# Optimization experiments

Hardware: AMD Instinct MI355X
Metric: run time of the kernel (lower is better)

## Reference

```python
import jax, jax.numpy as jnp
import numpy as np

IN_CH, OUT_CH, KH, KW = 512, 512, 3, 3
LR_MULT = 1.0
WEIGHT_SCALE = LR_MULT / np.sqrt(IN_CH * KH * KW)


def setup_inputs() -> dict:
    key = jax.random.key(0)
    k1, k2, k3 = jax.random.split(key, 3)
    x = jax.random.normal(k1, (16, IN_CH, 32, 32), dtype=jnp.float32)
    s = jax.random.normal(k2, (16, IN_CH), dtype=jnp.float32)
    weight = jax.random.normal(k3, (OUT_CH, IN_CH, KH, KW), dtype=jnp.float32) / LR_MULT
    return {"x": x, "s": s, "weight": weight}


def reference(x, s, weight):
    B, Cin, H, Wd = x.shape
    Cout = weight.shape[0]
    W = weight * WEIGHT_SCALE                          # [Cout, Cin, kH, kW]
    # per-sample modulation: [B, Cout, Cin, kH, kW]
    Wm = s[:, None, :, None, None] * W[None]
    # demodulation: normalize each (b, out_channel) filter
    sigma = jnp.sqrt(jnp.sum(Wm ** 2, axis=(-3, -2, -1), keepdims=True) + 1e-8)
    Wm = Wm / sigma
    # grouped conv with groups = B
    x_g = x.reshape(1, B * Cin, H, Wd)
    W_g = Wm.reshape(B * Cout, Cin, KH, KW)
    out = jax.lax.conv_general_dilated(
        x_g, W_g,
        window_strides=(1, 1),
        padding="SAME",
        rhs_dilation=(1, 1),
        feature_group_count=B,
        dimension_numbers=("NCHW", "OIHW", "NCHW"),
    )
    return out.reshape(B, Cout, out.shape[-2], out.shape[-1])
```

## Files before the change

kernel.cpp:

```cpp
#include <hip/hip_runtime.h>
#include <hip/hip_bf16.h>


typedef __attribute__((ext_vector_type(4))) float f32x4;
typedef __attribute__((ext_vector_type(8))) short bf16x8;

#define NB    16
#define CIN   512
#define COUT  512
#define KTOT  4608
#define NPIX  (NB * 32 * 32)
#define BUFELEM 24576

#define WAITV6() asm volatile("s_waitcnt vmcnt(6)" ::: "memory")
#define WAITV0() asm volatile("s_waitcnt vmcnt(0)" ::: "memory")
#define FENCE()  asm volatile("" ::: "memory")
#define BAR()    { FENCE(); __builtin_amdgcn_s_barrier(); FENCE(); }

__device__ __forceinline__ void gload_lds16(const void* g, void* l) {
  __builtin_amdgcn_global_load_lds(
      (__attribute__((address_space(1))) void*)(g),
      (__attribute__((address_space(3))) void*)(l), 16, 0, 0);
}

__global__ __launch_bounds__(256) void pack_w_kernel(
    const float* __restrict__ w, __hip_bfloat16* __restrict__ wB,
    float* __restrict__ wsq) {
  const int idx = blockIdx.x * 256 + threadIdx.x;
  const int o = idx >> 9, ci = idx & 511;
  const float* wp = w + (size_t)idx * 9;
  const float WSCALE = 0.014731391274719739f;
  float sum = 0.f;
#pragma unroll
  for (int t = 0; t < 9; ++t) {
    float v = wp[t] * WSCALE;
    sum += v * v;
    wB[(size_t)o * KTOT + t * 512 + ci] = __float2bfloat16(v);
  }
  wsq[idx] = sum;
}

__global__ __launch_bounds__(256) void calc_rsig_kernel(
    const float* __restrict__ s, const float* __restrict__ wsq,
    float* __restrict__ rsig) {
  const int wid = blockIdx.x * 4 + (threadIdx.x >> 6);
  const int lane = threadIdx.x & 63;
  const int b = wid >> 9, o = wid & 511;
  const float* sp = s + b * 512;
  const float* wp = wsq + o * 512;
  float sum = 0.f;
#pragma unroll
  for (int i = 0; i < 8; ++i) {
    float sv = sp[lane + i * 64];
    sum += sv * sv * wp[lane + i * 64];
  }
#pragma unroll
  for (int off = 32; off > 0; off >>= 1) sum += __shfl_down(sum, off, 64);
  if (lane == 0) rsig[wid] = 1.0f / sqrtf(sum + 1e-8f);
}

__global__ __launch_bounds__(256) void modulate_kernel(
    const float* __restrict__ x, const float* __restrict__ s,
    __hip_bfloat16* __restrict__ xpad) {
  const int by = blockIdx.x;
  const int b = by >> 5, y = by & 31;
  __shared__ __attribute__((aligned(16))) __hip_bfloat16 tile[32][72];
  const int tid = threadIdx.x;
  const int xc = tid & 31;
  const int cr0 = tid >> 5;
  const float* xrow = x + ((size_t)b * 512 * 32 + y) * 32;
  const float* sb = s + b * 512;
  __hip_bfloat16* orow = xpad + (size_t)((b * 34 + y + 1) * 34) * 512;

  for (int ci0 = 0; ci0 < 512; ci0 += 64) {
#pragma unroll
    for (int r = 0; r < 8; ++r) {
      const int cir = r * 8 + cr0;
      const int ci = ci0 + cir;
      float v = xrow[(size_t)ci * 1024 + xc] * sb[ci];
      tile[xc][cir] = __float2bfloat16(v);
    }
    __syncthreads();
    const int xcw = tid >> 3, vec = tid & 7;
    bf16x8 v = *(const bf16x8*)&tile[xcw][vec * 8];
    *(bf16x8*)(orow + (size_t)(xcw + 1) * 512 + ci0 + vec * 8) = v;
    __syncthreads();
  }
}

__global__ __launch_bounds__(512, 1) void conv_gemm_kernel(
    const __hip_bfloat16* __restrict__ wB,
    const __hip_bfloat16* __restrict__ xpad,
    const float* __restrict__ rsig,
    float* __restrict__ out) {
  extern __shared__ __attribute__((aligned(16))) __hip_bfloat16 lds[];

  const int tid = threadIdx.x;
  const int wv = tid >> 6, lane = tid & 63;
  const int bo0 = blockIdx.y << 7;
  const int bp0 = blockIdx.x << 8;
  const int wr = wv >> 2, wc = wv & 3;

  int gA[2];
#pragma unroll
  for (int r = 0; r < 2; ++r) {
    const int c = r * 512 + tid, row = c >> 3, sc = (c & 7) ^ (row & 7);
    gA[r] = (bo0 + row) * KTOT + sc * 8;
  }
  int gB[4];
#pragma unroll
  for (int r = 0; r < 4; ++r) {
    const int c = r * 512 + tid, row = c >> 3, sc = (c & 7) ^ (row & 7);
    const int p = bp0 + row, b = p >> 10, rem = p & 1023, y = rem >> 5,
              xx = rem & 31;
    gB[r] = ((b * 34 + y) * 34 + xx) * 512 + sc * 8;
  }

  auto stageA = [&](int kt2, int r) {
    __hip_bfloat16* dst = lds + (kt2 % 3) * BUFELEM + (size_t)(r * 512 + (wv << 6)) * 8;
    gload_lds16(wB + (size_t)(gA[r] + (kt2 << 6)), dst);
  };
  auto stageB = [&](int kt2, int r, int xoff) {
    __hip_bfloat16* dst = lds + (kt2 % 3) * BUFELEM + 8192 + (size_t)(r * 512 + (wv << 6)) * 8;
    gload_lds16(xpad + (size_t)(gB[r] + xoff), dst);
  };

  f32x4 acc[4][4];
#pragma unroll
  for (int mi = 0; mi < 4; ++mi)
#pragma unroll
    for (int ni = 0; ni < 4; ++ni) acc[mi][ni] = f32x4{0.f, 0.f, 0.f, 0.f};

  stageA(0, 0); stageA(0, 1);
  stageB(0, 0, 0); stageB(0, 1, 0); stageB(0, 2, 0); stageB(0, 3, 0);
  stageA(1, 0); stageA(1, 1);
  stageB(1, 0, 64); stageB(1, 1, 64); stageB(1, 2, 64); stageB(1, 3, 64);
  WAITV6();
  BAR();

  for (int kt = 0; kt < 72; ++kt) {
    const __hip_bfloat16* bufA = lds + (kt % 3) * BUFELEM;
    const __hip_bfloat16* bufB = bufA + 8192;
    const int kt2 = kt + 2;
    const bool pf = kt2 < 72;
    int xoff = 0;
    if (pf) {
      const int tap = kt2 >> 3, ty = (tap * 11) >> 5;
      xoff = (tap + 31 * ty) * 512 + ((kt2 & 7) << 6);
    }

    {
      bf16x8 af[4], bv[4];
      const int kb = (lane >> 4) << 4;
#pragma unroll
      for (int mi = 0; mi < 4; ++mi) {
        const int row = (wr << 6) + (mi << 4) + (lane & 15);
        af[mi] = *(const bf16x8*)((const char*)bufA + row * 128 +
                                  (kb ^ ((row & 7) << 4)));
      }
#pragma unroll
      for (int ni = 0; ni < 4; ++ni) {
        const int row = (wc << 6) + (ni << 4) + (lane & 15);
        bv[ni] = *(const bf16x8*)((const char*)bufB + row * 128 +
                                  (kb ^ ((row & 7) << 4)));
      }
      if (pf) { stageA(kt2, 0); stageA(kt2, 1); stageB(kt2, 0, xoff); }
      BAR();
      __builtin_amdgcn_s_setprio(1);
#pragma unroll
      for (int mi = 0; mi < 4; ++mi)
#pragma unroll
        for (int ni = 0; ni < 4; ++ni)
          acc[mi][ni] = __builtin_amdgcn_mfma_f32_16x16x32_bf16(
              af[mi], bv[ni], acc[mi][ni], 0, 0, 0);
      __builtin_amdgcn_s_setprio(0);
      BAR();
    }

    {
      bf16x8 af[4], bv[4];
      const int kb = 64 + ((lane >> 4) << 4);
#pragma unroll
      for (int mi = 0; mi < 4; ++mi) {
        const int row = (wr << 6) + (mi << 4) + (lane & 15);
        af[mi] = *(const bf16x8*)((const char*)bufA + row * 128 +
                                  (kb ^ ((row & 7) << 4)));
      }
#pragma unroll
      for (int ni = 0; ni < 4; ++ni) {
        const int row = (wc << 6) + (ni << 4) + (lane & 15);
        bv[ni] = *(const bf16x8*)((const char*)bufB + row * 128 +
                                  (kb ^ ((row & 7) << 4)));
      }
      if (pf) { stageB(kt2, 1, xoff); stageB(kt2, 2, xoff); stageB(kt2, 3, xoff); }
      BAR();
      __builtin_amdgcn_s_setprio(1);
#pragma unroll
      for (int mi = 0; mi < 4; ++mi)
#pragma unroll
        for (int ni = 0; ni < 4; ++ni)
          acc[mi][ni] = __builtin_amdgcn_mfma_f32_16x16x32_bf16(
              af[mi], bv[ni], acc[mi][ni], 0, 0, 0);
      __builtin_amdgcn_s_setprio(0);
      if (kt < 70) { WAITV6(); } else if (kt == 70) { WAITV0(); }
      BAR();
    }
  }

  const int bimg = bp0 >> 10;
#pragma unroll
  for (int mi = 0; mi < 4; ++mi) {
    const int o = bo0 + (wr << 6) + (mi << 4) + ((lane >> 4) << 2);
    const f32x4 rs = *(const f32x4*)(rsig + (bimg << 9) + o);
#pragma unroll
    for (int ni = 0; ni < 4; ++ni) {
      const int p = bp0 + (wc << 6) + (ni << 4) + (lane & 15);
      const int prem = p & 1023;
#pragma unroll
      for (int r = 0; r < 4; ++r)
        out[((size_t)(bimg << 9) + o + r) * 1024 + prem] =
            acc[mi][ni][r] * rs[r];
    }
  }
}

extern "C" void kernel_launch(void* const* d_in, const int* in_sizes, int n_in,
                              void* d_out, int out_size, void* d_ws,
                              size_t ws_size, hipStream_t stream) {
  const float* x = (const float*)d_in[0];
  const float* s = (const float*)d_in[1];
  const float* w = (const float*)d_in[2];
  float* out = (float*)d_out;

  char* ws = (char*)d_ws;
  const size_t xpad_bytes = (size_t)NB * 34 * 34 * 512 * 2;
  const size_t wB_bytes = (size_t)COUT * KTOT * 2;
  const size_t wsq_bytes = (size_t)COUT * CIN * 4;
  __hip_bfloat16* xpad = (__hip_bfloat16*)ws;
  __hip_bfloat16* wB = (__hip_bfloat16*)(ws + xpad_bytes);
  float* wsq = (float*)(ws + xpad_bytes + wB_bytes);
  float* rsig = (float*)(ws + xpad_bytes + wB_bytes + wsq_bytes);

  const int lds_bytes = 3 * BUFELEM * 2;
  hipFuncSetAttribute((const void*)conv_gemm_kernel,
                      hipFuncAttributeMaxDynamicSharedMemorySize, lds_bytes);

  hipMemsetAsync(xpad, 0, xpad_bytes, stream);
  pack_w_kernel<<<(COUT * CIN) / 256, 256, 0, stream>>>(w, wB, wsq);
  modulate_kernel<<<NB * 32, 256, 0, stream>>>(x, s, xpad);
  calc_rsig_kernel<<<(NB * COUT) / 4, 256, 0, stream>>>(s, wsq, rsig);
  conv_gemm_kernel<<<dim3(NPIX / 256, COUT / 128), 512, lds_bytes, stream>>>(
      wB, xpad, rsig, out);
}
```

Baseline: 108.9 us.

## Split GEMM k-tile into four quadrant phases with interleaved LDS reads and prefetch

Each k-tile iteration of the conv GEMM is restructured from two half-K phases into four output-quadrant phases. Each phase loads both K halves of the fragments it needs, issues part of the next tile's global-to-LDS prefetch, then waits on lgkmcnt and runs its MFMAs behind a scheduling barrier. The aim is to overlap LDS fragment reads and prefetch issue with MFMA work at finer granularity. Launch bounds also change to request two blocks per CU, which caps registers even though LDS use likely still allows only one block; this adds barriers per iteration and risks register spills.

```diff
diff --git a/kernel.cpp b/kernel.cpp
--- a/kernel.cpp
+++ b/kernel.cpp
@@ -10,10 +10,13 @@
 #define COUT  512
 #define KTOT  4608
 #define NPIX  (NB * 32 * 32)
+#define KTILES 72
 #define BUFELEM 24576
 
 #define WAITV6() asm volatile("s_waitcnt vmcnt(6)" ::: "memory")
 #define WAITV0() asm volatile("s_waitcnt vmcnt(0)" ::: "memory")
+#define LGKM0()  asm volatile("s_waitcnt lgkmcnt(0)" ::: "memory")
+#define SCHED0() __builtin_amdgcn_sched_barrier(0)
 #define FENCE()  asm volatile("" ::: "memory")
 #define BAR()    { FENCE(); __builtin_amdgcn_s_barrier(); FENCE(); }
 
@@ -88,7 +91,7 @@
   }
 }
 
-__global__ __launch_bounds__(512, 1) void conv_gemm_kernel(
+__global__ __launch_bounds__(512, 2) void conv_gemm_kernel(
     const __hip_bfloat16* __restrict__ wB,
     const __hip_bfloat16* __restrict__ xpad,
     const float* __restrict__ rsig,
@@ -138,73 +141,103 @@
   WAITV6();
   BAR();
 
-  for (int kt = 0; kt < 72; ++kt) {
+#pragma unroll 1
+  for (int kt = 0; kt < KTILES; ++kt) {
     const __hip_bfloat16* bufA = lds + (kt % 3) * BUFELEM;
     const __hip_bfloat16* bufB = bufA + 8192;
     const int kt2 = kt + 2;
-    const bool pf = kt2 < 72;
+    const bool pf = kt2 < KTILES;
     int xoff = 0;
     if (pf) {
-      const int tap = kt2 >> 3, ty = (tap * 11) >> 5;
-      xoff = (tap + 31 * ty) * 512 + ((kt2 & 7) << 6);
-    }
-
-    {
-      bf16x8 af[4], bv[4];
-      const int kb = (lane >> 4) << 4;
-#pragma unroll
-      for (int mi = 0; mi < 4; ++mi) {
-        const int row = (wr << 6) + (mi << 4) + (lane & 15);
-        af[mi] = *(const bf16x8*)((const char*)bufA + row * 128 +
-                                  (kb ^ ((row & 7) << 4)));
-      }
-#pragma unroll
-      for (int ni = 0; ni < 4; ++ni) {
-        const int row = (wc << 6) + (ni << 4) + (lane & 15);
-        bv[ni] = *(const bf16x8*)((const char*)bufB + row * 128 +
-                                  (kb ^ ((row & 7) << 4)));
-      }
-      if (pf) { stageA(kt2, 0); stageA(kt2, 1); stageB(kt2, 0, xoff); }
-      BAR();
-      __builtin_amdgcn_s_setprio(1);
-#pragma unroll
-      for (int mi = 0; mi < 4; ++mi)
-#pragma unroll
-        for (int ni = 0; ni < 4; ++ni)
-          acc[mi][ni] = __builtin_amdgcn_mfma_f32_16x16x32_bf16(
-              af[mi], bv[ni], acc[mi][ni], 0, 0, 0);
-      __builtin_amdgcn_s_setprio(0);
-      BAR();
-    }
-
-    {
-      bf16x8 af[4], bv[4];
-      const int kb = 64 + ((lane >> 4) << 4);
-#pragma unroll
-      for (int mi = 0; mi < 4; ++mi) {
-        const int row = (wr << 6) + (mi << 4) + (lane & 15);
-        af[mi] = *(const bf16x8*)((const char*)bufA + row * 128 +
-                                  (kb ^ ((row & 7) << 4)));
-      }
-#pragma unroll
-      for (int ni = 0; ni < 4; ++ni) {
-        const int row = (wc << 6) + (ni << 4) + (lane & 15);
-        bv[ni] = *(const bf16x8*)((const char*)bufB + row * 128 +
-                                  (kb ^ ((row & 7) << 4)));
-      }
-      if (pf) { stageB(kt2, 1, xoff); stageB(kt2, 2, xoff); stageB(kt2, 3, xoff); }
-      BAR();
-      __builtin_amdgcn_s_setprio(1);
-#pragma unroll
-      for (int mi = 0; mi < 4; ++mi)
-#pragma unroll
-        for (int ni = 0; ni < 4; ++ni)
-          acc[mi][ni] = __builtin_amdgcn_mfma_f32_16x16x32_bf16(
-              af[mi], bv[ni], acc[mi][ni], 0, 0, 0);
-      __builtin_amdgcn_s_setprio(0);
-      if (kt < 70) { WAITV6(); } else if (kt == 70) { WAITV0(); }
-      BAR();
-    }
+      const int tap = kt2 >> 3;
+      xoff = (tap + 31 * (tap / 3)) * 512 + ((kt2 & 7) << 6);
+    }
+
+    bf16x8 af[4][2], bv[4][2];
+    const int kbase = (lane >> 4) << 4;
+
+#pragma unroll
+    for (int mi = 0; mi < 2; ++mi) {
+      const int row = (wr << 6) + (mi << 4) + (lane & 15);
+      const int swz = (row & 7) << 4;
+      af[mi][0] = *(const bf16x8*)((const char*)bufA + row * 128 + (kbase ^ swz));
+      af[mi][1] = *(const bf16x8*)((const char*)bufA + row * 128 + ((64 | kbase) ^ swz));
+    }
+#pragma unroll
+    for (int ni = 0; ni < 2; ++ni) {
+      const int row = (wc << 6) + (ni << 4) + (lane & 15);
+      const int swz = (row & 7) << 4;
+      bv[ni][0] = *(const bf16x8*)((const char*)bufB + row * 128 + (kbase ^ swz));
+      bv[ni][1] = *(const bf16x8*)((const char*)bufB + row * 128 + ((64 | kbase) ^ swz));
+    }
+    if (pf) { stageA(kt2, 0); stageA(kt2, 1); }
+    BAR(); LGKM0(); SCHED0();
+    __builtin_amdgcn_s_setprio(1);
+#pragma unroll
+    for (int mi = 0; mi < 2; ++mi)
+#pragma unroll
+      for (int ni = 0; ni < 2; ++ni)
+#pragma unroll
+        for (int kk = 0; kk < 2; ++kk)
+          acc[mi][ni] = __builtin_amdgcn_mfma_f32_16x16x32_bf16(
+              af[mi][kk], bv[ni][kk], acc[mi][ni], 0, 0, 0);
+    __builtin_amdgcn_s_setprio(0);
+    BAR();
+
+#pragma unroll
+    for (int ni = 2; ni < 4; ++ni) {
+      const int row = (wc << 6) + (ni << 4) + (lane & 15);
+      const int swz = (row & 7) << 4;
+      bv[ni][0] = *(const bf16x8*)((const char*)bufB + row * 128 + (kbase ^ swz));
+      bv[ni][1] = *(const bf16x8*)((const char*)bufB + row * 128 + ((64 | kbase) ^ swz));
+    }
+    if (pf) { stageB(kt2, 0, xoff); stageB(kt2, 1, xoff); }
+    BAR(); LGKM0(); SCHED0();
+    __builtin_amdgcn_s_setprio(1);
+#pragma unroll
+    for (int mi = 0; mi < 2; ++mi)
+#pragma unroll
+      for (int ni = 2; ni < 4; ++ni)
+#pragma unroll
+        for (int kk = 0; kk < 2; ++kk)
+          acc[mi][ni] = __builtin_amdgcn_mfma_f32_16x16x32_bf16(
+              af[mi][kk], bv[ni][kk], acc[mi][ni], 0, 0, 0);
+    __builtin_amdgcn_s_setprio(0);
+    BAR();
+
+#pragma unroll
+    for (int mi = 2; mi < 4; ++mi) {
+      const int row = (wr << 6) + (mi << 4) + (lane & 15);
+      const int swz = (row & 7) << 4;
+      af[mi][0] = *(const bf16x8*)((const char*)bufA + row * 128 + (kbase ^ swz));
+      af[mi][1] = *(const bf16x8*)((const char*)bufA + row * 128 + ((64 | kbase) ^ swz));
+    }
+    if (pf) { stageB(kt2, 2, xoff); stageB(kt2, 3, xoff); }
+    BAR(); LGKM0(); SCHED0();
+    __builtin_amdgcn_s_setprio(1);
+#pragma unroll
+    for (int mi = 2; mi < 4; ++mi)
+#pragma unroll
+      for (int ni = 2; ni < 4; ++ni)
+#pragma unroll
+        for (int kk = 0; kk < 2; ++kk)
+          acc[mi][ni] = __builtin_amdgcn_mfma_f32_16x16x32_bf16(
+              af[mi][kk], bv[ni][kk], acc[mi][ni], 0, 0, 0);
+    __builtin_amdgcn_s_setprio(0);
+    BAR();
+
+    __builtin_amdgcn_s_setprio(1);
+#pragma unroll
+    for (int mi = 2; mi < 4; ++mi)
+#pragma unroll
+      for (int ni = 0; ni < 2; ++ni)
+#pragma unroll
+        for (int kk = 0; kk < 2; ++kk)
+          acc[mi][ni] = __builtin_amdgcn_mfma_f32_16x16x32_bf16(
+              af[mi][kk], bv[ni][kk], acc[mi][ni], 0, 0, 0);
+    __builtin_amdgcn_s_setprio(0);
+    if (kt < KTILES - 2) { WAITV6(); } else if (kt == KTILES - 2) { WAITV0(); }
+    BAR();
   }
 
   const int bimg = bp0 >> 10;
```

Result: slower. 114.1 us (+4.8%).

## Reuse haloed input tile across 3x3 taps with split-K waves and LDS reduction

Applied to the files above, without the earlier changes.

The conv GEMM now loads a haloed 10x34-pixel input tile per 64-channel group once into LDS and reuses it for all nine taps by shifting row indices, instead of re-fetching input for each tap. Weights are repacked channel-group-major so each tap's 64-wide weight slice is contiguous. Waves are split along K, each covering 128 pixels with 8 accumulator tiles, and partial sums are reduced through LDS before the epilogue. The changes cut global input traffic, but LDS grows to 144KB and register pressure rises, while the launch bounds hint now asks for two blocks per CU.

```diff
diff --git a/kernel.cpp b/kernel.cpp
--- a/kernel.cpp
+++ b/kernel.cpp
@@ -10,9 +10,9 @@
 #define COUT  512
 #define KTOT  4608
 #define NPIX  (NB * 32 * 32)
-#define BUFELEM 24576
-
-#define WAITV6() asm volatile("s_waitcnt vmcnt(6)" ::: "memory")
+
+#define WAITV8() asm volatile("s_waitcnt vmcnt(8)" ::: "memory")
+#define WAITV2() asm volatile("s_waitcnt vmcnt(2)" ::: "memory")
 #define WAITV0() asm volatile("s_waitcnt vmcnt(0)" ::: "memory")
 #define FENCE()  asm volatile("" ::: "memory")
 #define BAR()    { FENCE(); __builtin_amdgcn_s_barrier(); FENCE(); }
@@ -24,7 +24,7 @@
 }
 
 __global__ __launch_bounds__(256) void pack_w_kernel(
-    const float* __restrict__ w, __hip_bfloat16* __restrict__ wB,
+    const float* __restrict__ w, __hip_bfloat16* __restrict__ wB2,
     float* __restrict__ wsq) {
   const int idx = blockIdx.x * 256 + threadIdx.x;
   const int o = idx >> 9, ci = idx & 511;
@@ -35,7 +35,8 @@
   for (int t = 0; t < 9; ++t) {
     float v = wp[t] * WSCALE;
     sum += v * v;
-    wB[(size_t)o * KTOT + t * 512 + ci] = __float2bfloat16(v);
+    wB2[(size_t)o * KTOT + (ci >> 6) * 576 + t * 64 + (ci & 63)] =
+        __float2bfloat16(v);
   }
   wsq[idx] = sum;
 }
@@ -88,18 +89,30 @@
   }
 }
 
-__global__ __launch_bounds__(512, 1) void conv_gemm_kernel(
-    const __hip_bfloat16* __restrict__ wB,
+__global__ __launch_bounds__(512, 2) void conv_gemm_kernel(
+    const __hip_bfloat16* __restrict__ wB2,
     const __hip_bfloat16* __restrict__ xpad,
     const float* __restrict__ rsig,
     float* __restrict__ out) {
-  extern __shared__ __attribute__((aligned(16))) __hip_bfloat16 lds[];
+  extern __shared__ __attribute__((aligned(16))) char ldsc[];
 
   const int tid = threadIdx.x;
   const int wv = tid >> 6, lane = tid & 63;
+  const int l15 = lane & 15;
   const int bo0 = blockIdx.y << 7;
   const int bp0 = blockIdx.x << 8;
-  const int wr = wv >> 2, wc = wv & 3;
+  const int bimg = blockIdx.x >> 2;
+  const int y0 = (blockIdx.x & 3) << 3;
+  const int wr = wv >> 2, wc = (wv >> 1) & 1, wk = wv & 1;
+  const int kb = (wk << 6) | ((lane >> 4) << 4);
+
+  f32x4 rs[4];
+#pragma unroll
+  for (int mi = 0; mi < 4; ++mi) {
+    rs[mi] = *(const f32x4*)(rsig + (bimg << 9) + bo0 + (wr << 6) + (mi << 4) +
+                             ((lane >> 4) << 2));
+    asm volatile("" ::"v"(rs[mi]));
+  }
 
   int gA[2];
 #pragma unroll
@@ -107,119 +120,114 @@
     const int c = r * 512 + tid, row = c >> 3, sc = (c & 7) ^ (row & 7);
     gA[r] = (bo0 + row) * KTOT + sc * 8;
   }
-  int gB[4];
-#pragma unroll
-  for (int r = 0; r < 4; ++r) {
-    const int c = r * 512 + tid, row = c >> 3, sc = (c & 7) ^ (row & 7);
-    const int p = bp0 + row, b = p >> 10, rem = p & 1023, y = rem >> 5,
-              xx = rem & 31;
-    gB[r] = ((b * 34 + y) * 34 + xx) * 512 + sc * 8;
-  }
-
-  auto stageA = [&](int kt2, int r) {
-    __hip_bfloat16* dst = lds + (kt2 % 3) * BUFELEM + (size_t)(r * 512 + (wv << 6)) * 8;
-    gload_lds16(wB + (size_t)(gA[r] + (kt2 << 6)), dst);
+  int gB[6];
+#pragma unroll
+  for (int r = 0; r < 6; ++r) {
+    const int u = r * 512 + tid;
+    int R = u >> 3; if (R > 339) R = 339;
+    const int sc = (u & 7) ^ (R & 7);
+    const int yl = R / 34, xl = R - yl * 34;
+    gB[r] = ((bimg * 34 + y0 + yl) * 34 + xl) * 512 + sc * 8;
+  }
+  int Rb[8];
+#pragma unroll
+  for (int ni = 0; ni < 8; ++ni) {
+    const int p = (wc << 7) + (ni << 4) + l15;
+    Rb[ni] = (p >> 5) * 34 + (p & 31);
+  }
+
+  auto stageA = [&](int bufi, int koff) {
+    char* dst = ldsc + bufi * 16384;
+#pragma unroll
+    for (int r = 0; r < 2; ++r)
+      gload_lds16(wB2 + (size_t)(gA[r] + koff), dst + (r * 512 + tid) * 16);
   };
-  auto stageB = [&](int kt2, int r, int xoff) {
-    __hip_bfloat16* dst = lds + (kt2 % 3) * BUFELEM + 8192 + (size_t)(r * 512 + (wv << 6)) * 8;
-    gload_lds16(xpad + (size_t)(gB[r] + xoff), dst);
+  auto stageB = [&](int gi) {
+    char* dst = ldsc + 49152 + (gi & 1) * 49152;
+#pragma unroll
+    for (int r = 0; r < 6; ++r)
+      gload_lds16(xpad + (size_t)(gB[r] + gi * 64), dst + (r * 512 + tid) * 16);
   };
 
-  f32x4 acc[4][4];
+  f32x4 acc[4][8];
 #pragma unroll
   for (int mi = 0; mi < 4; ++mi)
 #pragma unroll
-    for (int ni = 0; ni < 4; ++ni) acc[mi][ni] = f32x4{0.f, 0.f, 0.f, 0.f};
-
-  stageA(0, 0); stageA(0, 1);
-  stageB(0, 0, 0); stageB(0, 1, 0); stageB(0, 2, 0); stageB(0, 3, 0);
-  stageA(1, 0); stageA(1, 1);
-  stageB(1, 0, 64); stageB(1, 1, 64); stageB(1, 2, 64); stageB(1, 3, 64);
-  WAITV6();
+    for (int ni = 0; ni < 8; ++ni) acc[mi][ni] = f32x4{0.f, 0.f, 0.f, 0.f};
+
+  stageB(0);
+  stageA(0, 0);
+  stageA(1, 64);
+  WAITV2();
   BAR();
 
-  for (int kt = 0; kt < 72; ++kt) {
-    const __hip_bfloat16* bufA = lds + (kt % 3) * BUFELEM;
-    const __hip_bfloat16* bufB = bufA + 8192;
-    const int kt2 = kt + 2;
-    const bool pf = kt2 < 72;
-    int xoff = 0;
-    if (pf) {
-      const int tap = kt2 >> 3, ty = (tap * 11) >> 5;
-      xoff = (tap + 31 * ty) * 512 + ((kt2 & 7) << 6);
-    }
-
-    {
-      bf16x8 af[4], bv[4];
-      const int kb = (lane >> 4) << 4;
+#pragma unroll 1
+  for (int g = 0; g < 8; ++g) {
+    const char* bufB = ldsc + 49152 + (g & 1) * 49152;
+#pragma unroll
+    for (int tap = 0; tap < 9; ++tap) {
+      if (tap == 0) { if (g < 7) stageB(g + 1); }
+      {
+        const int t2 = (tap < 7) ? tap + 2 : tap - 7;
+        const bool have = (tap <= 6) || (g < 7);
+        if (have) {
+          const int g2 = (tap < 7) ? g : g + 1;
+          stageA((tap + 2) % 3, g2 * 576 + t2 * 64);
+        }
+      }
+      const char* bufA = ldsc + (tap % 3) * 16384;
+      const int TY = tap / 3, TX = tap % 3;
+      bf16x8 av[4], bv[8];
 #pragma unroll
       for (int mi = 0; mi < 4; ++mi) {
-        const int row = (wr << 6) + (mi << 4) + (lane & 15);
-        af[mi] = *(const bf16x8*)((const char*)bufA + row * 128 +
-                                  (kb ^ ((row & 7) << 4)));
-      }
-#pragma unroll
-      for (int ni = 0; ni < 4; ++ni) {
-        const int row = (wc << 6) + (ni << 4) + (lane & 15);
-        bv[ni] = *(const bf16x8*)((const char*)bufB + row * 128 +
-                                  (kb ^ ((row & 7) << 4)));
-      }
-      if (pf) { stageA(kt2, 0); stageA(kt2, 1); stageB(kt2, 0, xoff); }
-      BAR();
+        const int row = (wr << 6) + (mi << 4) + l15;
+        av[mi] = *(const bf16x8*)(bufA + row * 128 + (kb ^ ((row & 7) << 4)));
+      }
+#pragma unroll
+      for (int ni = 0; ni < 8; ++ni) {
+        const int R = Rb[ni] + TY * 34 + TX;
+        bv[ni] = *(const bf16x8*)(bufB + R * 128 + (kb ^ ((R & 7) << 4)));
+      }
       __builtin_amdgcn_s_setprio(1);
 #pragma unroll
       for (int mi = 0; mi < 4; ++mi)
 #pragma unroll
-        for (int ni = 0; ni < 4; ++ni)
+        for (int ni = 0; ni < 8; ++ni)
           acc[mi][ni] = __builtin_amdgcn_mfma_f32_16x16x32_bf16(
-              af[mi], bv[ni], acc[mi][ni], 0, 0, 0);
+              av[mi], bv[ni], acc[mi][ni], 0, 0, 0);
       __builtin_amdgcn_s_setprio(0);
+      if (tap == 0)      { if (g < 7) { WAITV8(); } else { WAITV2(); } }
+      else if (tap >= 7) { if (g < 7) { WAITV2(); } else { WAITV0(); } }
+      else               { WAITV2(); }
       BAR();
     }
-
-    {
-      bf16x8 af[4], bv[4];
-      const int kb = 64 + ((lane >> 4) << 4);
-#pragma unroll
-      for (int mi = 0; mi < 4; ++mi) {
-        const int row = (wr << 6) + (mi << 4) + (lane & 15);
-        af[mi] = *(const bf16x8*)((const char*)bufA + row * 128 +
-                                  (kb ^ ((row & 7) << 4)));
-      }
-#pragma unroll
-      for (int ni = 0; ni < 4; ++ni) {
-        const int row = (wc << 6) + (ni << 4) + (lane & 15);
-        bv[ni] = *(const bf16x8*)((const char*)bufB + row * 128 +
-                                  (kb ^ ((row & 7) << 4)));
-      }
-      if (pf) { stageB(kt2, 1, xoff); stageB(kt2, 2, xoff); stageB(kt2, 3, xoff); }
-      BAR();
-      __builtin_amdgcn_s_setprio(1);
-#pragma unroll
-      for (int mi = 0; mi < 4; ++mi)
-#pragma unroll
-        for (int ni = 0; ni < 4; ++ni)
-          acc[mi][ni] = __builtin_amdgcn_mfma_f32_16x16x32_bf16(
-              af[mi], bv[ni], acc[mi][ni], 0, 0, 0);
-      __builtin_amdgcn_s_setprio(0);
-      if (kt < 70) { WAITV6(); } else if (kt == 70) { WAITV0(); }
-      BAR();
-    }
-  }
-
-  const int bimg = bp0 >> 10;
-#pragma unroll
-  for (int mi = 0; mi < 4; ++mi) {
-    const int o = bo0 + (wr << 6) + (mi << 4) + ((lane >> 4) << 2);
-    const f32x4 rs = *(const f32x4*)(rsig + (bimg << 9) + o);
-#pragma unroll
-    for (int ni = 0; ni < 4; ++ni) {
-      const int p = bp0 + (wc << 6) + (ni << 4) + (lane & 15);
-      const int prem = p & 1023;
-#pragma unroll
-      for (int r = 0; r < 4; ++r)
-        out[((size_t)(bimg << 9) + o + r) * 1024 + prem] =
-            acc[mi][ni][r] * rs[r];
+  }
+
+  const int slot = ((wr << 1) | wc) << 15;
+  if (wk) {
+#pragma unroll
+    for (int mi = 0; mi < 4; ++mi)
+#pragma unroll
+      for (int ni = 0; ni < 8; ++ni)
+        *(f32x4*)(ldsc + slot + (((mi << 3) | ni) << 10) + (lane << 4)) =
+            acc[mi][ni];
+  }
+  __syncthreads();
+  if (!wk) {
+#pragma unroll
+    for (int mi = 0; mi < 4; ++mi) {
+      const int o = bo0 + (wr << 6) + (mi << 4) + ((lane >> 4) << 2);
+#pragma unroll
+      for (int ni = 0; ni < 8; ++ni) {
+        const f32x4 o4 =
+            *(const f32x4*)(ldsc + slot + (((mi << 3) | ni) << 10) + (lane << 4));
+        const f32x4 a = acc[mi][ni] + o4;
+        const int p = bp0 + (wc << 7) + (ni << 4) + l15;
+        const int prem = p & 1023;
+#pragma unroll
+        for (int r = 0; r < 4; ++r)
+          out[((size_t)(bimg << 9) + o + r) * 1024 + prem] = a[r] * rs[mi][r];
+      }
     }
   }
 }
@@ -237,18 +245,18 @@
   const size_t wB_bytes = (size_t)COUT * KTOT * 2;
   const size_t wsq_bytes = (size_t)COUT * CIN * 4;
   __hip_bfloat16* xpad = (__hip_bfloat16*)ws;
-  __hip_bfloat16* wB = (__hip_bfloat16*)(ws + xpad_bytes);
+  __hip_bfloat16* wB2 = (__hip_bfloat16*)(ws + xpad_bytes);
   float* wsq = (float*)(ws + xpad_bytes + wB_bytes);
   float* rsig = (float*)(ws + xpad_bytes + wB_bytes + wsq_bytes);
 
-  const int lds_bytes = 3 * BUFELEM * 2;
+  const int lds_bytes = 147456;
   hipFuncSetAttribute((const void*)conv_gemm_kernel,
                       hipFuncAttributeMaxDynamicSharedMemorySize, lds_bytes);
 
   hipMemsetAsync(xpad, 0, xpad_bytes, stream);
-  pack_w_kernel<<<(COUT * CIN) / 256, 256, 0, stream>>>(w, wB, wsq);
+  pack_w_kernel<<<(COUT * CIN) / 256, 256, 0, stream>>>(w, wB2, wsq);
   modulate_kernel<<<NB * 32, 256, 0, stream>>>(x, s, xpad);
   calc_rsig_kernel<<<(NB * COUT) / 4, 256, 0, stream>>>(s, wsq, rsig);
   conv_gemm_kernel<<<dim3(NPIX / 256, COUT / 128), 512, lds_bytes, stream>>>(
-      wB, xpad, rsig, out);
-}
+      wB2, xpad, rsig, out);
+}
```

After: 266.4 us. 145% more time.
